# Performance work log

Hardware: AMD Instinct MI355X
Metric: run time of the kernel (lower is better)

The kernel has to match this reference:

```python
import jax, jax.numpy as jnp
import numpy as np

NUM_LEVELS = 4
RADIUS = 4


def _bilinear_zeros(img, x, y):
    # img: (N, Hl, Wl); x, y: (N, K) pixel coords (align_corners=True identity map).
    # Replicates F.grid_sample(mode='bilinear', padding_mode='zeros', align_corners=True).
    N, Hl, Wl = img.shape
    x0 = jnp.floor(x); y0 = jnp.floor(y)
    wx1 = x - x0; wx0 = 1.0 - wx1
    wy1 = y - y0; wy0 = 1.0 - wy1
    bidx = jnp.arange(N)[:, None]

    def gather(xi, yi):
        inb = (xi >= 0) & (xi <= Wl - 1) & (yi >= 0) & (yi <= Hl - 1)
        xc = jnp.clip(xi, 0, Wl - 1).astype(jnp.int32)
        yc = jnp.clip(yi, 0, Hl - 1).astype(jnp.int32)
        vals = img[bidx, yc, xc]
        return jnp.where(inb, vals, jnp.zeros((), img.dtype))

    return (wy0 * wx0 * gather(x0, y0) + wy0 * wx1 * gather(x0 + 1, y0)
            + wy1 * wx0 * gather(x0, y0 + 1) + wy1 * wx1 * gather(x0 + 1, y0 + 1))


def setup_inputs() -> dict:
    key = jax.random.key(0)
    k1, k2, k3 = jax.random.split(key, 3)
    B, C, H, W = 2, 256, 64, 64
    fmap1 = jax.random.normal(k1, (B, C, H, W), dtype=jnp.float32)
    fmap2 = jax.random.normal(k2, (B, C, H, W), dtype=jnp.float32)
    # coords = base pixel grid + small random flow (stays mostly in-bounds)
    ys, xs = jnp.meshgrid(jnp.arange(H, dtype=jnp.float32), jnp.arange(W, dtype=jnp.float32), indexing='ij')
    grid = jnp.stack([xs, ys], axis=0)[None]  # (1, 2, H, W), channel0 = x
    flow = (jax.random.uniform(k3, (B, 2, H, W), dtype=jnp.float32) - 0.5) * 20.0
    coords = grid + flow
    return {'fmap1': fmap1, 'fmap2': fmap2, 'coords': coords}


def reference(fmap1, fmap2, coords):
    B, C, H, W = fmap1.shape
    HW = H * W
    # all-pairs correlation: (B, HW, HW), scaled by 1/sqrt(C)
    corr = jnp.einsum('bci,bcj->bij', fmap1.reshape(B, C, HW), fmap2.reshape(B, C, HW))
    corr = corr / jnp.sqrt(jnp.asarray(C, fmap1.dtype))
    corr = corr.reshape(B * HW, H, W)
    pyramid = [corr]
    for _ in range(NUM_LEVELS - 1):
        N, Hl, Wl = corr.shape
        corr = corr.reshape(N, Hl // 2, 2, Wl // 2, 2).mean(axis=(2, 4))  # avg_pool2d(2,2)
        pyramid.append(corr)

    r = RADIUS
    dy = jnp.linspace(-r, r, 2 * r + 1, dtype=coords.dtype)
    dx = jnp.linspace(-r, r, 2 * r + 1, dtype=coords.dtype)
    gy, gx = jnp.meshgrid(dy, dx, indexing='ij')  # matches torch.meshgrid(dy, dx)
    d0 = gy.reshape(-1); d1 = gx.reshape(-1)      # K = (2r+1)^2

    cperm = coords.transpose(0, 2, 3, 1).reshape(B * HW, 2)  # (N, 2), [:,0]=x, [:,1]=y
    outs = []
    for i, corr_l in enumerate(pyramid):
        cl = cperm / (2.0 ** i)
        # coords_lvl = centroid + delta; xgrid uses delta[...,0]=dy grid, ygrid uses delta[...,1]=dx grid
        x = cl[:, 0:1] + d0[None, :]
        y = cl[:, 1:2] + d1[None, :]
        outs.append(_bilinear_zeros(corr_l, x, y))  # (N, K)
    out = jnp.concatenate(outs, axis=-1)            # (N, num_levels*K)
    out = out.reshape(B, H, W, -1).transpose(0, 3, 1, 2)  # (B, 324, H, W)
    return out
```

## Files before the change

kernel.cpp:

```cpp
#include <hip/hip_runtime.h>
#include <cstdint>

#define B2 2
#define CCH 256
#define HH 64
#define WW 64
#define HWHW 4096
#define KOUT 324

typedef _Float16 half_t;
typedef _Float16 h2 __attribute__((ext_vector_type(2)));

#if !__has_builtin(__builtin_amdgcn_fdot2)
#define NO_FDOT2 1
#endif

__device__ __forceinline__ float fdot2f(h2 a, h2 b, float c) {
#ifdef NO_FDOT2
  return c + (float)a.x * (float)b.x + (float)a.y * (float)b.y;
#else
  return __builtin_amdgcn_fdot2(a, b, c, false);
#endif
}

__global__ __launch_bounds__(256) void transpose_cl(
    const float* __restrict__ f1, const float* __restrict__ f2,
    half_t* __restrict__ f1t, half_t* __restrict__ f2t) {
  __shared__ float tile[32][33];
  int zz = blockIdx.z;
  const float* src = (zz < 2) ? f1 : f2;
  half_t* dst = (zz < 2) ? f1t : f2t;
  float s = (zz < 2) ? 0.0625f : 1.0f;
  int b = zz & 1;
  int hw0 = blockIdx.x * 32;
  int c0 = blockIdx.y * 32;
  int tx = threadIdx.x;
  int ty = threadIdx.y;
  const float* sb = src + (size_t)b * CCH * HWHW;
  half_t* db = dst + (size_t)b * HWHW * CCH;
#pragma unroll
  for (int i = 0; i < 4; i++)
    tile[ty + i * 8][tx] = sb[(size_t)(c0 + ty + i * 8) * HWHW + hw0 + tx];
  __syncthreads();
#pragma unroll
  for (int i = 0; i < 4; i++)
    db[(size_t)(hw0 + ty + i * 8) * CCH + c0 + tx] = (half_t)(tile[tx][ty + i * 8] * s);
}

__global__ __launch_bounds__(256) void pool_all(
    const h2* __restrict__ l0, h2* __restrict__ l1,
    h2* __restrict__ l2, h2* __restrict__ l3) {
  int idx = blockIdx.x * blockDim.x + threadIdx.x;
  const int n1 = B2 * 32 * 32 * 128;
  const int n2 = B2 * 16 * 16 * 128;
  const int n3 = B2 * 8 * 8 * 128;
  int L, Wo, local;
  h2* dst;
  if (idx < n1) { L = 1; Wo = 32; local = idx; dst = l1; }
  else if (idx < n1 + n2) { L = 2; Wo = 16; local = idx - n1; dst = l2; }
  else if (idx < n1 + n2 + n3) { L = 3; Wo = 8; local = idx - n1 - n2; dst = l3; }
  else return;
  int f = 1 << L;
  int sh = 6 - L;
  int c2 = local & 127;
  int t = local >> 7;
  int x = t & (Wo - 1);
  int y = (t >> sh) & (Wo - 1);
  int b = t >> (2 * sh);
  const h2* src = l0 + (size_t)b * HWHW * 128 + c2;
  float ax = 0.f, ay = 0.f;
  for (int dy = 0; dy < f; dy++)
    for (int dx = 0; dx < f; dx++) {
      h2 a = src[(size_t)((y * f + dy) * WW + (x * f + dx)) * 128];
      ax += (float)a.x; ay += (float)a.y;
    }
  float s = 1.0f / (float)(f * f);
  h2 r;
  r.x = (half_t)(ax * s);
  r.y = (half_t)(ay * s);
  dst[local] = r;
}

__device__ __forceinline__ float dpp_sum16(float x) {
  int v;
  v = __builtin_amdgcn_update_dpp(0, __float_as_int(x), 0xB1, 0xF, 0xF, true);
  x += __int_as_float(v);
  v = __builtin_amdgcn_update_dpp(0, __float_as_int(x), 0x4E, 0xF, 0xF, true);
  x += __int_as_float(v);
  v = __builtin_amdgcn_update_dpp(0, __float_as_int(x), 0x141, 0xF, 0xF, true);
  x += __int_as_float(v);
  v = __builtin_amdgcn_update_dpp(0, __float_as_int(x), 0x140, 0xF, 0xF, true);
  x += __int_as_float(v);
  return x;
}

__global__ __launch_bounds__(256) void sample_k(
    const float* __restrict__ coords,
    const half_t* __restrict__ f1t,
    const half_t* __restrict__ f2l0, const half_t* __restrict__ f2l1,
    const half_t* __restrict__ f2l2, const half_t* __restrict__ f2l3,
    float* __restrict__ pout) {
  __shared__ float4 f1s4[32];
  __shared__ float P[4][100];
  int bid = blockIdx.x;
  int n = ((bid & 7) << 10) | (bid >> 3);
  int b = n >> 12;
  int i = n & 4095;
  int tid = threadIdx.x;
  if (tid < 32) f1s4[tid] = ((const float4*)(f1t + (size_t)n * CCH))[tid];
  float clx = coords[(size_t)(b * 2 + 0) * HWHW + i];
  float cly = coords[(size_t)(b * 2 + 1) * HWHW + i];
  __syncthreads();

  int l = tid >> 6;
  int lane = tid & 63;
  int lg = lane >> 4;
  int l16 = lane & 15;

  float inv = 1.0f / (float)(1 << l);
  float xl = clx * inv, yl = cly * inv;
  float fx = floorf(xl), fy = floorf(yl);
  int ix0 = (int)fx - 4, iy0 = (int)fy - 4;
  float wx1 = xl - fx, wx0 = 1.0f - wx1;
  float wy1 = yl - fy, wy0 = 1.0f - wy1;
  int Hl = HH >> l, Wl = WW >> l;
  const half_t* f2 = (l == 0) ? f2l0 : (l == 1) ? f2l1 : (l == 2) ? f2l2 : f2l3;
  const float4* f2b = (const float4*)(f2) + (size_t)b * Hl * Wl * 32 + l16;

  const h2* f1h = (const h2*)f1s4;
  h2 fa0 = f1h[l16 * 4 + 0], fa1 = f1h[l16 * 4 + 1];
  h2 fa2 = f1h[l16 * 4 + 2], fa3 = f1h[l16 * 4 + 3];
  h2 fb0 = f1h[64 + l16 * 4 + 0], fb1 = f1h[64 + l16 * 4 + 1];
  h2 fb2 = f1h[64 + l16 * 4 + 2], fb3 = f1h[64 + l16 * 4 + 3];

  int u = 0, v = lg, t = lg;
  for (int it = 0; it < 25; it++) {
    int txp = ix0 + u, typ = iy0 + v;
    bool inb = ((unsigned)txp < (unsigned)Wl) & ((unsigned)typ < (unsigned)Hl);
    float d = 0.0f;
    if (inb) {
      const float4* tp = f2b + (size_t)(typ * Wl + txp) * 32;
      float4 A = tp[0];
      float4 Bv = tp[16];
      const h2* ah = (const h2*)&A;
      const h2* bh = (const h2*)&Bv;
      d = fdot2f(ah[0], fa0, d);
      d = fdot2f(ah[1], fa1, d);
      d = fdot2f(ah[2], fa2, d);
      d = fdot2f(ah[3], fa3, d);
      d = fdot2f(bh[0], fb0, d);
      d = fdot2f(bh[1], fb1, d);
      d = fdot2f(bh[2], fb2, d);
      d = fdot2f(bh[3], fb3, d);
    }
    d = dpp_sum16(d);
    if (l16 == 0) P[l][t] = d;
    t += 4;
    v += 4;
    bool wrap = v >= 10;
    v = wrap ? v - 10 : v;
    u = wrap ? u + 1 : u;
  }
  __syncthreads();

  float* po = pout + (size_t)n * KOUT + l * 81;
  {
    int k = lane;
    int a = k / 9, bb = k - a * 9;
    float val = wy0 * (wx0 * P[l][a * 10 + bb] + wx1 * P[l][(a + 1) * 10 + bb])
              + wy1 * (wx0 * P[l][a * 10 + bb + 1] + wx1 * P[l][(a + 1) * 10 + bb + 1]);
    po[k] = val;
  }
  if (lane < 17) {
    int k = lane + 64;
    int a = k / 9, bb = k - a * 9;
    float val = wy0 * (wx0 * P[l][a * 10 + bb] + wx1 * P[l][(a + 1) * 10 + bb])
              + wy1 * (wx0 * P[l][a * 10 + bb + 1] + wx1 * P[l][(a + 1) * 10 + bb + 1]);
    po[k] = val;
  }
}

__global__ __launch_bounds__(256) void writeout(
    const float* __restrict__ pout, float* __restrict__ out) {
  __shared__ float tile[32][33];
  int b = blockIdx.z;
  int hw0 = blockIdx.x * 32;
  int ch0 = blockIdx.y * 32;
  int tx = threadIdx.x, ty = threadIdx.y;
  const float* pb = pout + (size_t)b * HWHW * KOUT;
  float* ob = out + (size_t)b * KOUT * HWHW;
  if (ch0 + tx < KOUT) {
#pragma unroll
    for (int i = 0; i < 4; i++)
      tile[ty + i * 8][tx] = pb[(size_t)(hw0 + ty + i * 8) * KOUT + ch0 + tx];
  }
  __syncthreads();
#pragma unroll
  for (int i = 0; i < 4; i++) {
    int ch = ch0 + ty + i * 8;
    if (ch < KOUT)
      ob[(size_t)ch * HWHW + hw0 + tx] = tile[tx][ty + i * 8];
  }
}

extern "C" void kernel_launch(void* const* d_in, const int* in_sizes, int n_in,
                              void* d_out, int out_size, void* d_ws, size_t ws_size,
                              hipStream_t stream) {
  const float* fmap1 = (const float*)d_in[0];
  const float* fmap2 = (const float*)d_in[1];
  const float* coords = (const float*)d_in[2];
  float* out = (float*)d_out;

  char* ws = (char*)d_ws;
  half_t* f1t  = (half_t*)(ws);
  half_t* f2l0 = (half_t*)(ws + ((size_t)4 << 20));
  half_t* f2l1 = (half_t*)(ws + ((size_t)8 << 20));
  half_t* f2l2 = (half_t*)(ws + ((size_t)9 << 20));
  half_t* f2l3 = (half_t*)(ws + ((size_t)9 << 20) + ((size_t)512 << 10));
  float*  pout = (float*)(ws + ((size_t)10 << 20));

  dim3 tb(32, 8, 1);
  dim3 tg(HWHW / 32, CCH / 32, 4);
  transpose_cl<<<tg, tb, 0, stream>>>(fmap1, fmap2, f1t, f2l0);

  int npool = B2 * (32 * 32 + 16 * 16 + 8 * 8) * 128;
  pool_all<<<(npool + 255) / 256, 256, 0, stream>>>(
      (const h2*)f2l0, (h2*)f2l1, (h2*)f2l2, (h2*)f2l3);

  sample_k<<<HWHW * B2, 256, 0, stream>>>(coords, f1t, f2l0, f2l1, f2l2, f2l3, pout);

  dim3 wb(32, 8, 1);
  dim3 wg(HWHW / 32, (KOUT + 31) / 32, B2);
  writeout<<<wg, wb, 0, stream>>>(pout, out);
}
```

Measured before the change: 147.7 us.

## Batch 16 pixels per block, stage level-3 map in LDS, write output directly

The sampling kernel now handles 16 consecutive pixels per 512-thread block instead of one pixel per 256-thread block. Each block caches the whole level-3 pyramid image for its batch item in shared memory. Results are written straight into the final channel-major output, which removes the intermediate pout buffer and the separate transpose/writeout kernel. This cuts a launch and a full round trip of the output through memory, but it greatly raises LDS use per block and leaves only 512 blocks, which may limit occupancy.

After: 154.7 us. 4.7% more time.

```diff
diff --git a/kernel.cpp b/kernel.cpp
--- a/kernel.cpp
+++ b/kernel.cpp
@@ -11,15 +11,11 @@
 typedef _Float16 half_t;
 typedef _Float16 h2 __attribute__((ext_vector_type(2)));
 
-#if !__has_builtin(__builtin_amdgcn_fdot2)
-#define NO_FDOT2 1
-#endif
-
 __device__ __forceinline__ float fdot2f(h2 a, h2 b, float c) {
-#ifdef NO_FDOT2
+#if __has_builtin(__builtin_amdgcn_fdot2)
+  return __builtin_amdgcn_fdot2(a, b, c, false);
+#else
   return c + (float)a.x * (float)b.x + (float)a.y * (float)b.y;
-#else
-  return __builtin_amdgcn_fdot2(a, b, c, false);
 #endif
 }
 
@@ -94,112 +90,135 @@
   return x;
 }
 
-__global__ __launch_bounds__(256) void sample_k(
+__global__ __launch_bounds__(512, 4) void sample16(
     const float* __restrict__ coords,
     const half_t* __restrict__ f1t,
     const half_t* __restrict__ f2l0, const half_t* __restrict__ f2l1,
     const half_t* __restrict__ f2l2, const half_t* __restrict__ f2l3,
-    float* __restrict__ pout) {
-  __shared__ float4 f1s4[32];
-  __shared__ float P[4][100];
+    float* __restrict__ out) {
+  __shared__ float4 f1s4[512];
+  __shared__ float4 l3img[2048];
+  __shared__ float P[4][16][100];
+  __shared__ float wgt[4][16][4];
+  __shared__ float cxy[2][16];
+
   int bid = blockIdx.x;
-  int n = ((bid & 7) << 10) | (bid >> 3);
-  int b = n >> 12;
-  int i = n & 4095;
+  int g = ((bid & 7) << 6) | (bid >> 3);
+  int n0 = g << 4;
+  int b = n0 >> 12;
+  int i0 = n0 & 4095;
+  int yi = i0 >> 6;
+  int x0 = i0 & 63;
   int tid = threadIdx.x;
-  if (tid < 32) f1s4[tid] = ((const float4*)(f1t + (size_t)n * CCH))[tid];
-  float clx = coords[(size_t)(b * 2 + 0) * HWHW + i];
-  float cly = coords[(size_t)(b * 2 + 1) * HWHW + i];
+
+  f1s4[tid] = ((const float4*)(f1t + (size_t)n0 * CCH))[tid];
+  {
+    const float4* l3g = (const float4*)(f2l3 + (size_t)b * 64 * CCH);
+#pragma unroll
+    for (int r = 0; r < 4; r++) l3img[tid + r * 512] = l3g[tid + r * 512];
+  }
+  if (tid < 32) {
+    int q = tid & 15, c = tid >> 4;
+    cxy[c][q] = coords[(size_t)(b * 2 + c) * HWHW + i0 + q];
+  }
   __syncthreads();
 
-  int l = tid >> 6;
+  int w = tid >> 6;
+  int l = w >> 1;
+  int h = w & 1;
   int lane = tid & 63;
   int lg = lane >> 4;
   int l16 = lane & 15;
 
   float inv = 1.0f / (float)(1 << l);
-  float xl = clx * inv, yl = cly * inv;
-  float fx = floorf(xl), fy = floorf(yl);
-  int ix0 = (int)fx - 4, iy0 = (int)fy - 4;
-  float wx1 = xl - fx, wx0 = 1.0f - wx1;
-  float wy1 = yl - fy, wy0 = 1.0f - wy1;
   int Hl = HH >> l, Wl = WW >> l;
-  const half_t* f2 = (l == 0) ? f2l0 : (l == 1) ? f2l1 : (l == 2) ? f2l2 : f2l3;
+  const half_t* f2 = (l == 0) ? f2l0 : (l == 1) ? f2l1 : f2l2;
   const float4* f2b = (const float4*)(f2) + (size_t)b * Hl * Wl * 32 + l16;
-
+  const float4* l3b = l3img + l16;
   const h2* f1h = (const h2*)f1s4;
-  h2 fa0 = f1h[l16 * 4 + 0], fa1 = f1h[l16 * 4 + 1];
-  h2 fa2 = f1h[l16 * 4 + 2], fa3 = f1h[l16 * 4 + 3];
-  h2 fb0 = f1h[64 + l16 * 4 + 0], fb1 = f1h[64 + l16 * 4 + 1];
-  h2 fb2 = f1h[64 + l16 * 4 + 2], fb3 = f1h[64 + l16 * 4 + 3];
-
-  int u = 0, v = lg, t = lg;
-  for (int it = 0; it < 25; it++) {
-    int txp = ix0 + u, typ = iy0 + v;
-    bool inb = ((unsigned)txp < (unsigned)Wl) & ((unsigned)typ < (unsigned)Hl);
-    float d = 0.0f;
-    if (inb) {
-      const float4* tp = f2b + (size_t)(typ * Wl + txp) * 32;
-      float4 A = tp[0];
-      float4 Bv = tp[16];
-      const h2* ah = (const h2*)&A;
-      const h2* bh = (const h2*)&Bv;
-      d = fdot2f(ah[0], fa0, d);
-      d = fdot2f(ah[1], fa1, d);
-      d = fdot2f(ah[2], fa2, d);
-      d = fdot2f(ah[3], fa3, d);
-      d = fdot2f(bh[0], fb0, d);
-      d = fdot2f(bh[1], fb1, d);
-      d = fdot2f(bh[2], fb2, d);
-      d = fdot2f(bh[3], fb3, d);
-    }
-    d = dpp_sum16(d);
-    if (l16 == 0) P[l][t] = d;
-    t += 4;
-    v += 4;
-    bool wrap = v >= 10;
-    v = wrap ? v - 10 : v;
-    u = wrap ? u + 1 : u;
+
+  for (int qq = 0; qq < 8; qq++) {
+    int q = h * 8 + qq;
+    float clx = cxy[0][q], cly = cxy[1][q];
+    float xl = clx * inv, yl = cly * inv;
+    float fx = floorf(xl), fy = floorf(yl);
+    int ix0 = (int)fx - 4, iy0 = (int)fy - 4;
+    float wx1 = xl - fx, wy1 = yl - fy;
+    if (lane == 0) {
+      wgt[l][q][0] = 1.0f - wx1; wgt[l][q][1] = wx1;
+      wgt[l][q][2] = 1.0f - wy1; wgt[l][q][3] = wy1;
+    }
+    int fi = q * 128 + l16 * 4;
+    h2 fa0 = f1h[fi + 0], fa1 = f1h[fi + 1], fa2 = f1h[fi + 2], fa3 = f1h[fi + 3];
+    h2 fb0 = f1h[fi + 64], fb1 = f1h[fi + 65], fb2 = f1h[fi + 66], fb3 = f1h[fi + 67];
+
+    int u = 0, v = lg, t = lg;
+    if (l == 3) {
+      for (int it = 0; it < 25; it++) {
+        int txp = ix0 + u, typ = iy0 + v;
+        bool inb = ((unsigned)txp < (unsigned)Wl) & ((unsigned)typ < (unsigned)Hl);
+        float d = 0.0f;
+        if (inb) {
+          const float4* tp = l3b + (size_t)(typ * 8 + txp) * 32;
+          float4 A = tp[0];
+          float4 Bv = tp[16];
+          const h2* ah = (const h2*)&A;
+          const h2* bh = (const h2*)&Bv;
+          d = fdot2f(ah[0], fa0, d); d = fdot2f(ah[1], fa1, d);
+          d = fdot2f(ah[2], fa2, d); d = fdot2f(ah[3], fa3, d);
+          d = fdot2f(bh[0], fb0, d); d = fdot2f(bh[1], fb1, d);
+          d = fdot2f(bh[2], fb2, d); d = fdot2f(bh[3], fb3, d);
+        }
+        d = dpp_sum16(d);
+        if (l16 == 0) P[l][q][t] = d;
+        t += 4; v += 4;
+        bool wrap = v >= 10;
+        v = wrap ? v - 10 : v;
+        u = wrap ? u + 1 : u;
+      }
+    } else {
+      for (int it = 0; it < 25; it++) {
+        int txp = ix0 + u, typ = iy0 + v;
+        bool inb = ((unsigned)txp < (unsigned)Wl) & ((unsigned)typ < (unsigned)Hl);
+        float d = 0.0f;
+        if (inb) {
+          const float4* tp = f2b + (size_t)(typ * Wl + txp) * 32;
+          float4 A = tp[0];
+          float4 Bv = tp[16];
+          const h2* ah = (const h2*)&A;
+          const h2* bh = (const h2*)&Bv;
+          d = fdot2f(ah[0], fa0, d); d = fdot2f(ah[1], fa1, d);
+          d = fdot2f(ah[2], fa2, d); d = fdot2f(ah[3], fa3, d);
+          d = fdot2f(bh[0], fb0, d); d = fdot2f(bh[1], fb1, d);
+          d = fdot2f(bh[2], fb2, d); d = fdot2f(bh[3], fb3, d);
+        }
+        d = dpp_sum16(d);
+        if (l16 == 0) P[l][q][t] = d;
+        t += 4; v += 4;
+        bool wrap = v >= 10;
+        v = wrap ? v - 10 : v;
+        u = wrap ? u + 1 : u;
+      }
+    }
   }
   __syncthreads();
 
-  float* po = pout + (size_t)n * KOUT + l * 81;
-  {
-    int k = lane;
-    int a = k / 9, bb = k - a * 9;
-    float val = wy0 * (wx0 * P[l][a * 10 + bb] + wx1 * P[l][(a + 1) * 10 + bb])
-              + wy1 * (wx0 * P[l][a * 10 + bb + 1] + wx1 * P[l][(a + 1) * 10 + bb + 1]);
-    po[k] = val;
-  }
-  if (lane < 17) {
-    int k = lane + 64;
-    int a = k / 9, bb = k - a * 9;
-    float val = wy0 * (wx0 * P[l][a * 10 + bb] + wx1 * P[l][(a + 1) * 10 + bb])
-              + wy1 * (wx0 * P[l][a * 10 + bb + 1] + wx1 * P[l][(a + 1) * 10 + bb + 1]);
-    po[k] = val;
-  }
-}
-
-__global__ __launch_bounds__(256) void writeout(
-    const float* __restrict__ pout, float* __restrict__ out) {
-  __shared__ float tile[32][33];
-  int b = blockIdx.z;
-  int hw0 = blockIdx.x * 32;
-  int ch0 = blockIdx.y * 32;
-  int tx = threadIdx.x, ty = threadIdx.y;
-  const float* pb = pout + (size_t)b * HWHW * KOUT;
-  float* ob = out + (size_t)b * KOUT * HWHW;
-  if (ch0 + tx < KOUT) {
-#pragma unroll
-    for (int i = 0; i < 4; i++)
-      tile[ty + i * 8][tx] = pb[(size_t)(hw0 + ty + i * 8) * KOUT + ch0 + tx];
-  }
-  __syncthreads();
-#pragma unroll
-  for (int i = 0; i < 4; i++) {
-    int ch = ch0 + ty + i * 8;
-    if (ch < KOUT)
-      ob[(size_t)ch * HWHW + hw0 + tx] = tile[tx][ty + i * 8];
+  int limit = h ? 40 : 41;
+#pragma unroll
+  for (int kk = 0; kk < 11; kk++) {
+    int idx = kk * 64 + lane;
+    int kl = idx >> 4;
+    int q = idx & 15;
+    if (kl < limit) {
+      int k = h * 41 + kl;
+      int a = k / 9, bb2 = k - a * 9;
+      float wx0 = wgt[l][q][0], wx1 = wgt[l][q][1];
+      float wy0 = wgt[l][q][2], wy1 = wgt[l][q][3];
+      const float* Pq = P[l][q];
+      float val = wy0 * (wx0 * Pq[a * 10 + bb2] + wx1 * Pq[(a + 1) * 10 + bb2])
+                + wy1 * (wx0 * Pq[a * 10 + bb2 + 1] + wx1 * Pq[(a + 1) * 10 + bb2 + 1]);
+      out[(size_t)(b * KOUT + l * 81 + k) * HWHW + (size_t)yi * WW + x0 + q] = val;
+    }
   }
 }
 
@@ -217,7 +236,6 @@
   half_t* f2l1 = (half_t*)(ws + ((size_t)8 << 20));
   half_t* f2l2 = (half_t*)(ws + ((size_t)9 << 20));
   half_t* f2l3 = (half_t*)(ws + ((size_t)9 << 20) + ((size_t)512 << 10));
-  float*  pout = (float*)(ws + ((size_t)10 << 20));
 
   dim3 tb(32, 8, 1);
   dim3 tg(HWHW / 32, CCH / 32, 4);
@@ -227,9 +245,5 @@
   pool_all<<<(npool + 255) / 256, 256, 0, stream>>>(
       (const h2*)f2l0, (h2*)f2l1, (h2*)f2l2, (h2*)f2l3);
 
-  sample_k<<<HWHW * B2, 256, 0, stream>>>(coords, f1t, f2l0, f2l1, f2l2, f2l3, pout);
-
-  dim3 wb(32, 8, 1);
-  dim3 wg(HWHW / 32, (KOUT + 31) / 32, B2);
-  writeout<<<wg, wb, 0, stream>>>(pout, out);
-}
+  sample16<<<512, 512, 0, stream>>>(coords, f1t, f2l0, f2l1, f2l2, f2l3, out);
+}
```
